# Kernel tuning notes

Hardware: AMD Instinct MI355X
Metric: run time of the kernel (lower is better)

The kernel has to match this reference:

```python
import jax, jax.numpy as jnp
import numpy as np

N_NODES = 100000
N_EDGES = 1600000
D_IN = 128
D_OUT = 128


def setup_inputs() -> dict:
    key = jax.random.key(0)
    ks = jax.random.split(key, 8)
    h = jax.random.normal(ks[0], (N_NODES, D_IN), dtype=jnp.float32)
    edge_val = jax.random.uniform(ks[1], (N_EDGES,), dtype=jnp.float32)
    # Linear weights in torch layout [out, in]
    W_self = jax.random.normal(ks[2], (D_OUT, D_IN), dtype=jnp.float32) * (1.0 / np.sqrt(D_IN))
    b_self = jax.random.normal(ks[3], (D_OUT,), dtype=jnp.float32) * 0.01
    W_nb = jax.random.normal(ks[4], (D_OUT, D_IN), dtype=jnp.float32) * (1.0 / np.sqrt(D_IN))
    b_nb = jax.random.normal(ks[5], (D_OUT,), dtype=jnp.float32) * 0.01
    edge_row = jax.random.randint(ks[6], (N_EDGES,), 0, N_NODES, dtype=jnp.int64)
    edge_col = jax.random.randint(ks[7], (N_EDGES,), 0, N_NODES, dtype=jnp.int64)
    return {"h": h, "edge_val": edge_val, "W_self": W_self, "b_self": b_self,
            "W_nb": W_nb, "b_nb": b_nb, "edge_row": edge_row, "edge_col": edge_col}


def reference(h, edge_val, W_self, b_self, W_nb, b_nb, edge_row, edge_col):
    # self_h = Linear_self(h[:out_nodes]); out_nodes == N_NODES here
    self_h = h @ W_self.T + b_self  # [N, D_OUT]
    # neighbor_h = adj.spmm(h): sparse COO (row, col, val) times dense h
    msgs = edge_val[:, None] * h[edge_col]            # [E, D_IN]
    neighbor_h = jax.ops.segment_sum(msgs, edge_row, num_segments=N_NODES)  # [N, D_IN]
    out = self_h + neighbor_h @ W_nb.T + b_nb
    return out
```

## Files before the change

kernel.cpp:

```cpp
#include <hip/hip_runtime.h>


constexpr int NN = 100000;
constexpr int NE = 1600000;
constexpr int D  = 128;
constexpr int NN_PAD = 100032;
constexpr int NBUCK  = 391;
constexpr int BCAP   = 4608;
constexpr int CHUNK  = 4096;
constexpr int NCH    = (NE + CHUNK - 1) / CHUNK;

typedef __bf16 bf16x8 __attribute__((ext_vector_type(8)));
typedef float  f32x4  __attribute__((ext_vector_type(4)));
typedef float  f32x2  __attribute__((ext_vector_type(2)));

__global__ __launch_bounds__(256) void gemm_mfma(
    const float* __restrict__ h,
    const float* __restrict__ Wself,
    const float* __restrict__ Wnb,
    const float* __restrict__ bself,
    const float* __restrict__ bnb,
    float* __restrict__ out,
    __bf16* __restrict__ tmpb)
{
    const int t    = threadIdx.x;
    const int w    = t >> 6;
    const int lane = t & 63;
    const int l15  = lane & 15;
    const int quad = lane >> 4;

    bf16x8 b[4][4];
    #pragma unroll
    for (int ns = 0; ns < 4; ++ns) {
        int wrow = w * 64 + ns * 16 + l15;
        const float* wr = (wrow < D) ? (Wself + (size_t)wrow * D)
                                     : (Wnb + (size_t)(wrow - D) * D);
        #pragma unroll
        for (int kk = 0; kk < 4; ++kk) {
            f32x4 lo = *(const f32x4*)(wr + kk * 32 + quad * 8);
            f32x4 hi = *(const f32x4*)(wr + kk * 32 + quad * 8 + 4);
            bf16x8 bb;
            #pragma unroll
            for (int j = 0; j < 4; ++j) { bb[j] = (__bf16)lo[j]; bb[4 + j] = (__bf16)hi[j]; }
            b[ns][kk] = bb;
        }
    }

    float bias[4];
    #pragma unroll
    for (int ns = 0; ns < 4; ++ns) {
        int col = w * 64 + ns * 16 + l15;
        bias[ns] = (col < D) ? (bself[col] + bnb[col]) : 0.f;
    }

    #pragma unroll
    for (int c = 0; c < 4; ++c) {
        const int m0 = blockIdx.x * 64 + c * 16;
        int arow = m0 + l15;
        if (arow >= NN) arow = NN - 1;
        const float* aptr = h + (size_t)arow * D + quad * 8;

        bf16x8 afr[4];
        #pragma unroll
        for (int kk = 0; kk < 4; ++kk) {
            f32x4 lo = *(const f32x4*)(aptr + kk * 32);
            f32x4 hi = *(const f32x4*)(aptr + kk * 32 + 4);
            bf16x8 a;
            #pragma unroll
            for (int j = 0; j < 4; ++j) { a[j] = (__bf16)lo[j]; a[4 + j] = (__bf16)hi[j]; }
            afr[kk] = a;
        }

        f32x4 acc[4];
        #pragma unroll
        for (int ns = 0; ns < 4; ++ns) acc[ns] = (f32x4){0.f, 0.f, 0.f, 0.f};
        #pragma unroll
        for (int ns = 0; ns < 4; ++ns)
            #pragma unroll
            for (int kk = 0; kk < 4; ++kk)
                acc[ns] = __builtin_amdgcn_mfma_f32_16x16x32_bf16(afr[kk], b[ns][kk], acc[ns], 0, 0, 0);

        if (w < 2) {
            #pragma unroll
            for (int ns = 0; ns < 4; ++ns) {
                int col = w * 64 + ns * 16 + l15;
                #pragma unroll
                for (int i = 0; i < 4; ++i) {
                    int row = m0 + quad * 4 + i;
                    if (row < NN) out[(size_t)row * D + col] = acc[ns][i] + bias[ns];
                }
            }
        } else {
            #pragma unroll
            for (int ns = 0; ns < 4; ++ns) {
                int col = w * 64 + ns * 16 + l15 - D;
                #pragma unroll
                for (int i = 0; i < 4; ++i) {
                    int row = m0 + quad * 4 + i;
                    if (row < NN) tmpb[(size_t)row * D + col] = (__bf16)acc[ns][i];
                }
            }
        }
    }
}

__global__ __launch_bounds__(256) void wc_scatter(
    const int* __restrict__ erow, const int* __restrict__ ecol,
    const float* __restrict__ eval_,
    int* __restrict__ gcount, int2* __restrict__ epair)
{
    __shared__ int  cnt[NBUCK];
    __shared__ int  lscan[NBUCK];
    __shared__ int  gbase[NBUCK];
    __shared__ int  ss[512];
    __shared__ int2 sbuf[CHUNK];
    __shared__ int  saddr[CHUNK];
    __shared__ int  s_total;

    const int t  = threadIdx.x;
    const int c0 = blockIdx.x * CHUNK;

    for (int b = t; b < NBUCK; b += 256) cnt[b] = 0;
    __syncthreads();

    int   bp[16];
    int   colr[16];
    float valr[16];
    #pragma unroll
    for (int j = 0; j < 16; ++j) {
        int e = c0 + j * 256 + t;
        if (e < NE) {
            int r   = erow[e];
            colr[j] = ecol[e];
            valr[j] = eval_[e];
            int b   = r >> 8;
            int pos = atomicAdd(&cnt[b], 1);
            bp[j]   = b | ((r & 255) << 9) | (pos << 17);
        } else bp[j] = -1;
    }
    __syncthreads();

    ss[t]       = (t < NBUCK)       ? cnt[t]       : 0;
    ss[t + 256] = (t + 256 < NBUCK) ? cnt[t + 256] : 0;
    __syncthreads();
    for (int off = 1; off < 512; off <<= 1) {
        int i0 = t, i1 = t + 256;
        int r0 = ss[i0] + ((i0 >= off) ? ss[i0 - off] : 0);
        int r1 = ss[i1] + ((i1 >= off) ? ss[i1 - off] : 0);
        __syncthreads();
        ss[i0] = r0; ss[i1] = r1;
        __syncthreads();
    }
    if (t < NBUCK) {
        int n = cnt[t];
        lscan[t] = ss[t] - n;
        gbase[t] = (n > 0) ? atomicAdd(&gcount[t], n) : 0;
    }
    if (t + 256 < NBUCK) {
        int n = cnt[t + 256];
        lscan[t + 256] = ss[t + 256] - n;
        gbase[t + 256] = (n > 0) ? atomicAdd(&gcount[t + 256], n) : 0;
    }
    if (t == 0) s_total = ss[511];
    __syncthreads();

    #pragma unroll
    for (int j = 0; j < 16; ++j) {
        if (bp[j] >= 0) {
            int b   = bp[j] & 511;
            int rlo = (bp[j] >> 9) & 255;
            int pos = bp[j] >> 17;
            int slot = lscan[b] + pos;
            sbuf[slot]  = make_int2(colr[j] | (rlo << 17), __float_as_int(valr[j]));
            saddr[slot] = b * BCAP + gbase[b] + pos;
        }
    }
    __syncthreads();

    int ce = s_total;
    for (int i = t; i < ce; i += 256)
        epair[saddr[i]] = sbuf[i];
}

__global__ __launch_bounds__(256) void bucket_sort(
    const int2* __restrict__ epair, const int* __restrict__ gcount,
    int2* __restrict__ epair2, int2* __restrict__ rowrange)
{
    __shared__ int  cnt[256];
    __shared__ int  off[256];
    __shared__ int  cur[256];
    __shared__ int  ss[256];
    __shared__ int2 sorted[BCAP];

    const int t = threadIdx.x;
    const int b = blockIdx.x;
    const int n = gcount[b];
    const int2* src = epair + (size_t)b * BCAP;

    cnt[t] = 0;
    __syncthreads();
    for (int i = t; i < n; i += 256)
        atomicAdd(&cnt[(src[i].x >> 17) & 255], 1);
    __syncthreads();

    int v = cnt[t];
    ss[t] = v;
    __syncthreads();
    for (int o = 1; o < 256; o <<= 1) {
        int y = (t >= o) ? ss[t - o] : 0;
        __syncthreads();
        ss[t] += y;
        __syncthreads();
    }
    off[t] = ss[t] - v;
    cur[t] = ss[t] - v;
    __syncthreads();

    for (int i = t; i < n; i += 256) {
        int2 p = src[i];
        int slot = atomicAdd(&cur[(p.x >> 17) & 255], 1);
        sorted[slot] = p;
    }
    __syncthreads();

    const int base = b * BCAP;
    for (int i = t; i < n; i += 256)
        epair2[base + i] = sorted[i];
    int row = b * 256 + t;
    if (row < NN)
        rowrange[row] = make_int2(base + off[t], base + off[t] + cnt[t]);
}

__global__ __launch_bounds__(256) void aggregate(
    const __bf16* __restrict__ tmpb, const int2* __restrict__ rowrange,
    const int2* __restrict__ epair2, float* __restrict__ out,
    int row0, int nrows)
{
    int wave = row0 + ((blockIdx.x * 256 + threadIdx.x) >> 6);
    if (wave >= row0 + nrows) return;
    int lane = threadIdx.x & 63;
    int2 rr = rowrange[wave];
    int beg = __builtin_amdgcn_readfirstlane(rr.x);
    int end = __builtin_amdgcn_readfirstlane(rr.y);

    float ax[4] = {0.f, 0.f, 0.f, 0.f};
    float ay[4] = {0.f, 0.f, 0.f, 0.f};
    int e = beg;
    for (; e + 3 < end; e += 4) {
        int2 p[4];
        #pragma unroll
        for (int k = 0; k < 4; ++k) p[k] = epair2[e + k];
        #pragma unroll
        for (int k = 0; k < 4; ++k) {
            int col = p[k].x & 0x1FFFF;
            unsigned u = *(const unsigned*)(tmpb + (size_t)col * D + lane * 2);
            float v = __int_as_float(p[k].y);
            ax[k] += v * __uint_as_float(u << 16);
            ay[k] += v * __uint_as_float(u & 0xffff0000u);
        }
    }
    for (; e < end; ++e) {
        int2 p = epair2[e];
        int col = p.x & 0x1FFFF;
        unsigned u = *(const unsigned*)(tmpb + (size_t)col * D + lane * 2);
        float v = __int_as_float(p.y);
        ax[0] += v * __uint_as_float(u << 16);
        ay[0] += v * __uint_as_float(u & 0xffff0000u);
    }
    f32x2* o = (f32x2*)(out + (size_t)wave * D + lane * 2);
    f32x2 c = __builtin_nontemporal_load(o);
    c.x += (ax[0] + ax[1]) + (ax[2] + ax[3]);
    c.y += (ay[0] + ay[1]) + (ay[2] + ay[3]);
    __builtin_nontemporal_store(c, o);
}

extern "C" void kernel_launch(void* const* d_in, const int* in_sizes, int n_in,
                              void* d_out, int out_size, void* d_ws, size_t ws_size,
                              hipStream_t stream) {
    const float* h     = (const float*)d_in[0];
    const float* eval_ = (const float*)d_in[1];
    const float* Wself = (const float*)d_in[2];
    const float* bself = (const float*)d_in[3];
    const float* Wnb   = (const float*)d_in[4];
    const float* bnb   = (const float*)d_in[5];
    const int*   erow  = (const int*)d_in[6];
    const int*   ecol  = (const int*)d_in[7];
    float* out = (float*)d_out;

    char* p = (char*)d_ws;
    __bf16* tmpb    = (__bf16*)p;   p += (size_t)NN_PAD * D * 2;
    int2*   epair   = (int2*)p;     p += (size_t)NBUCK * BCAP * 8;
    int2*   epair2  = (int2*)p;     p += (size_t)NBUCK * BCAP * 8;
    int2*   rowrange= (int2*)p;     p += (size_t)NN * 8;
    int*    gcount  = (int*)p;

    hipMemsetAsync(gcount, 0, NBUCK * 4, stream);

    gemm_mfma<<<NN_PAD / 64, 256, 0, stream>>>(h, Wself, Wnb, bself, bnb, out, tmpb);
    wc_scatter<<<NCH, 256, 0, stream>>>(erow, ecol, eval_, gcount, epair);
    bucket_sort<<<NBUCK, 256, 0, stream>>>(epair, gcount, epair2, rowrange);
    aggregate<<<(50000 * 64) / 256, 256, 0, stream>>>(tmpb, rowrange, epair2, out, 0, 50000);
    aggregate<<<(50000 * 64) / 256, 256, 0, stream>>>(tmpb, rowrange, epair2, out, 50000, 50000);
}
```

Measured before the change: 278.5 us.

## Stage GEMM A-tile in LDS and widen scatter/sort kernels to 512 threads

The GEMM kernel now loads each 64-row tile of h once, converts it to bf16 and stores it in shared memory. Previously each of the 4 waves read and converted the same rows from global memory. The edge scatter and bucket sort kernels move to 512-thread blocks, and bucket sort keeps its edge pairs in registers so it reads the global buffer once instead of twice. The costs are more LDS per GEMM block and more registers (a dynamically indexed register array in bucket_sort), which may hurt occupancy or spill.

```diff
diff --git a/kernel.cpp b/kernel.cpp
--- a/kernel.cpp
+++ b/kernel.cpp
@@ -4,11 +4,13 @@
 constexpr int NN = 100000;
 constexpr int NE = 1600000;
 constexpr int D  = 128;
-constexpr int NN_PAD = 100032;
 constexpr int NBUCK  = 391;
 constexpr int BCAP   = 4608;
 constexpr int CHUNK  = 4096;
 constexpr int NCH    = (NE + CHUNK - 1) / CHUNK;
+constexpr int GM     = 64;
+constexpr int NGB    = (NN + GM - 1) / GM;
+constexpr int LP     = 132;
 
 typedef __bf16 bf16x8 __attribute__((ext_vector_type(8)));
 typedef float  f32x4  __attribute__((ext_vector_type(4)));
@@ -23,11 +25,26 @@
     float* __restrict__ out,
     __bf16* __restrict__ tmpb)
 {
+    __shared__ __bf16 hs[GM * LP];
     const int t    = threadIdx.x;
     const int w    = t >> 6;
     const int lane = t & 63;
     const int l15  = lane & 15;
     const int quad = lane >> 4;
+    const int row0 = blockIdx.x * GM;
+
+    #pragma unroll
+    for (int it = 0; it < 4; ++it) {
+        int idx = it * 2048 + t * 8;
+        int r = idx >> 7, c = idx & 127;
+        int gr = row0 + r; if (gr >= NN) gr = NN - 1;
+        f32x4 lo = *(const f32x4*)(h + (size_t)gr * D + c);
+        f32x4 hi = *(const f32x4*)(h + (size_t)gr * D + c + 4);
+        bf16x8 v;
+        #pragma unroll
+        for (int j = 0; j < 4; ++j) { v[j] = (__bf16)lo[j]; v[4 + j] = (__bf16)hi[j]; }
+        *(bf16x8*)(hs + r * LP + c) = v;
+    }
 
     bf16x8 b[4][4];
     #pragma unroll
@@ -45,49 +62,43 @@
             b[ns][kk] = bb;
         }
     }
-
     float bias[4];
     #pragma unroll
     for (int ns = 0; ns < 4; ++ns) {
         int col = w * 64 + ns * 16 + l15;
         bias[ns] = (col < D) ? (bself[col] + bnb[col]) : 0.f;
     }
-
-    #pragma unroll
-    for (int c = 0; c < 4; ++c) {
-        const int m0 = blockIdx.x * 64 + c * 16;
-        int arow = m0 + l15;
-        if (arow >= NN) arow = NN - 1;
-        const float* aptr = h + (size_t)arow * D + quad * 8;
-
+    __syncthreads();
+
+    f32x4 acc[4][4];
+    #pragma unroll
+    for (int mi = 0; mi < 4; ++mi)
+        #pragma unroll
+        for (int ns = 0; ns < 4; ++ns) acc[mi][ns] = (f32x4){0.f, 0.f, 0.f, 0.f};
+
+    #pragma unroll
+    for (int mi = 0; mi < 4; ++mi) {
         bf16x8 afr[4];
         #pragma unroll
-        for (int kk = 0; kk < 4; ++kk) {
-            f32x4 lo = *(const f32x4*)(aptr + kk * 32);
-            f32x4 hi = *(const f32x4*)(aptr + kk * 32 + 4);
-            bf16x8 a;
-            #pragma unroll
-            for (int j = 0; j < 4; ++j) { a[j] = (__bf16)lo[j]; a[4 + j] = (__bf16)hi[j]; }
-            afr[kk] = a;
-        }
-
-        f32x4 acc[4];
-        #pragma unroll
-        for (int ns = 0; ns < 4; ++ns) acc[ns] = (f32x4){0.f, 0.f, 0.f, 0.f};
+        for (int kk = 0; kk < 4; ++kk)
+            afr[kk] = *(const bf16x8*)(hs + (mi * 16 + l15) * LP + quad * 8 + kk * 32);
         #pragma unroll
         for (int ns = 0; ns < 4; ++ns)
             #pragma unroll
             for (int kk = 0; kk < 4; ++kk)
-                acc[ns] = __builtin_amdgcn_mfma_f32_16x16x32_bf16(afr[kk], b[ns][kk], acc[ns], 0, 0, 0);
-
+                acc[mi][ns] = __builtin_amdgcn_mfma_f32_16x16x32_bf16(afr[kk], b[ns][kk], acc[mi][ns], 0, 0, 0);
+    }
+
+    #pragma unroll
+    for (int mi = 0; mi < 4; ++mi) {
         if (w < 2) {
             #pragma unroll
             for (int ns = 0; ns < 4; ++ns) {
                 int col = w * 64 + ns * 16 + l15;
                 #pragma unroll
                 for (int i = 0; i < 4; ++i) {
-                    int row = m0 + quad * 4 + i;
-                    if (row < NN) out[(size_t)row * D + col] = acc[ns][i] + bias[ns];
+                    int row = row0 + mi * 16 + quad * 4 + i;
+                    if (row < NN) out[(size_t)row * D + col] = acc[mi][ns][i] + bias[ns];
                 }
             }
         } else {
@@ -96,15 +107,15 @@
                 int col = w * 64 + ns * 16 + l15 - D;
                 #pragma unroll
                 for (int i = 0; i < 4; ++i) {
-                    int row = m0 + quad * 4 + i;
-                    if (row < NN) tmpb[(size_t)row * D + col] = (__bf16)acc[ns][i];
+                    int row = row0 + mi * 16 + quad * 4 + i;
+                    if (row < NN) tmpb[(size_t)row * D + col] = (__bf16)acc[mi][ns][i];
                 }
             }
         }
     }
 }
 
-__global__ __launch_bounds__(256) void wc_scatter(
+__global__ __launch_bounds__(512) void wc_scatter(
     const int* __restrict__ erow, const int* __restrict__ ecol,
     const float* __restrict__ eval_,
     int* __restrict__ gcount, int2* __restrict__ epair)
@@ -120,15 +131,15 @@
     const int t  = threadIdx.x;
     const int c0 = blockIdx.x * CHUNK;
 
-    for (int b = t; b < NBUCK; b += 256) cnt[b] = 0;
-    __syncthreads();
-
-    int   bp[16];
-    int   colr[16];
-    float valr[16];
-    #pragma unroll
-    for (int j = 0; j < 16; ++j) {
-        int e = c0 + j * 256 + t;
+    for (int b = t; b < NBUCK; b += 512) cnt[b] = 0;
+    __syncthreads();
+
+    int   bp[8];
+    int   colr[8];
+    float valr[8];
+    #pragma unroll
+    for (int j = 0; j < 8; ++j) {
+        int e = c0 + j * 512 + t;
         if (e < NE) {
             int r   = erow[e];
             colr[j] = ecol[e];
@@ -140,15 +151,12 @@
     }
     __syncthreads();
 
-    ss[t]       = (t < NBUCK)       ? cnt[t]       : 0;
-    ss[t + 256] = (t + 256 < NBUCK) ? cnt[t + 256] : 0;
+    ss[t] = (t < NBUCK) ? cnt[t] : 0;
     __syncthreads();
     for (int off = 1; off < 512; off <<= 1) {
-        int i0 = t, i1 = t + 256;
-        int r0 = ss[i0] + ((i0 >= off) ? ss[i0 - off] : 0);
-        int r1 = ss[i1] + ((i1 >= off) ? ss[i1 - off] : 0);
+        int y = (t >= off) ? ss[t - off] : 0;
         __syncthreads();
-        ss[i0] = r0; ss[i1] = r1;
+        ss[t] += y;
         __syncthreads();
     }
     if (t < NBUCK) {
@@ -156,16 +164,11 @@
         lscan[t] = ss[t] - n;
         gbase[t] = (n > 0) ? atomicAdd(&gcount[t], n) : 0;
     }
-    if (t + 256 < NBUCK) {
-        int n = cnt[t + 256];
-        lscan[t + 256] = ss[t + 256] - n;
-        gbase[t + 256] = (n > 0) ? atomicAdd(&gcount[t + 256], n) : 0;
-    }
     if (t == 0) s_total = ss[511];
     __syncthreads();
 
     #pragma unroll
-    for (int j = 0; j < 16; ++j) {
+    for (int j = 0; j < 8; ++j) {
         if (bp[j] >= 0) {
             int b   = bp[j] & 511;
             int rlo = (bp[j] >> 9) & 255;
@@ -178,16 +181,16 @@
     __syncthreads();
 
     int ce = s_total;
-    for (int i = t; i < ce; i += 256)
+    for (int i = t; i < ce; i += 512)
         epair[saddr[i]] = sbuf[i];
 }
 
-__global__ __launch_bounds__(256) void bucket_sort(
+__global__ __launch_bounds__(512) void bucket_sort(
     const int2* __restrict__ epair, const int* __restrict__ gcount,
     int2* __restrict__ epair2, int2* __restrict__ rowrange)
 {
     __shared__ int  cnt[256];
-    __shared__ int  off[256];
+    __shared__ int  off2[256];
     __shared__ int  cur[256];
     __shared__ int  ss[256];
     __shared__ int2 sorted[BCAP];
@@ -197,38 +200,48 @@
     const int n = gcount[b];
     const int2* src = epair + (size_t)b * BCAP;
 
-    cnt[t] = 0;
-    __syncthreads();
-    for (int i = t; i < n; i += 256)
-        atomicAdd(&cnt[(src[i].x >> 17) & 255], 1);
-    __syncthreads();
-
-    int v = cnt[t];
-    ss[t] = v;
+    if (t < 256) cnt[t] = 0;
+    __syncthreads();
+
+    int2 r[9];
+    int  nr = 0;
+    for (int i = t; i < n; i += 512) {
+        int2 p = src[i];
+        r[nr++] = p;
+        atomicAdd(&cnt[(p.x >> 17) & 255], 1);
+    }
+    __syncthreads();
+
+    if (t < 256) ss[t] = cnt[t];
     __syncthreads();
     for (int o = 1; o < 256; o <<= 1) {
-        int y = (t >= o) ? ss[t - o] : 0;
+        int y = 0;
+        if (t < 256 && t >= o) y = ss[t - o];
         __syncthreads();
-        ss[t] += y;
+        if (t < 256) ss[t] += y;
         __syncthreads();
     }
-    off[t] = ss[t] - v;
-    cur[t] = ss[t] - v;
-    __syncthreads();
-
-    for (int i = t; i < n; i += 256) {
-        int2 p = src[i];
-        int slot = atomicAdd(&cur[(p.x >> 17) & 255], 1);
-        sorted[slot] = p;
+    if (t < 256) {
+        int v = cnt[t];
+        off2[t] = ss[t] - v;
+        cur[t]  = ss[t] - v;
+    }
+    __syncthreads();
+
+    for (int j = 0; j < nr; ++j) {
+        int slot = atomicAdd(&cur[(r[j].x >> 17) & 255], 1);
+        sorted[slot] = r[j];
     }
     __syncthreads();
 
     const int base = b * BCAP;
-    for (int i = t; i < n; i += 256)
+    for (int i = t; i < n; i += 512)
         epair2[base + i] = sorted[i];
-    int row = b * 256 + t;
-    if (row < NN)
-        rowrange[row] = make_int2(base + off[t], base + off[t] + cnt[t]);
+    if (t < 256) {
+        int row = b * 256 + t;
+        if (row < NN)
+            rowrange[row] = make_int2(base + off2[t], base + off2[t] + cnt[t]);
+    }
 }
 
 __global__ __launch_bounds__(256) void aggregate(
@@ -288,7 +301,7 @@
     float* out = (float*)d_out;
 
     char* p = (char*)d_ws;
-    __bf16* tmpb    = (__bf16*)p;   p += (size_t)NN_PAD * D * 2;
+    __bf16* tmpb    = (__bf16*)p;   p += (size_t)NGB * GM * D * 2;
     int2*   epair   = (int2*)p;     p += (size_t)NBUCK * BCAP * 8;
     int2*   epair2  = (int2*)p;     p += (size_t)NBUCK * BCAP * 8;
     int2*   rowrange= (int2*)p;     p += (size_t)NN * 8;
@@ -296,9 +309,9 @@
 
     hipMemsetAsync(gcount, 0, NBUCK * 4, stream);
 
-    gemm_mfma<<<NN_PAD / 64, 256, 0, stream>>>(h, Wself, Wnb, bself, bnb, out, tmpb);
-    wc_scatter<<<NCH, 256, 0, stream>>>(erow, ecol, eval_, gcount, epair);
-    bucket_sort<<<NBUCK, 256, 0, stream>>>(epair, gcount, epair2, rowrange);
+    gemm_mfma<<<NGB, 256, 0, stream>>>(h, Wself, Wnb, bself, bnb, out, tmpb);
+    wc_scatter<<<NCH, 512, 0, stream>>>(erow, ecol, eval_, gcount, epair);
+    bucket_sort<<<NBUCK, 512, 0, stream>>>(epair, gcount, epair2, rowrange);
     aggregate<<<(50000 * 64) / 256, 256, 0, stream>>>(tmpb, rowrange, epair2, out, 0, 50000);
     aggregate<<<(50000 * 64) / 256, 256, 0, stream>>>(tmpb, rowrange, epair2, out, 50000, 50000);
 }
```

After: 265.0 us. 1.05x faster.
